# Performance work log

Measured on AMD Instinct MI355X. Metric: run time of the kernel, lower is better.

Reference implementation:

```python
import jax, jax.numpy as jnp
import numpy as np

NEG_SLOPE = 0.2
EPS = 1e-16

N_NODES = 50000
N_EDGES = 800000
IN_DIM = 64
HEADS = 4
HEAD_DIM = 64


def setup_inputs() -> dict:
    key = jax.random.key(0)
    k1, k2, k3, k4, k5 = jax.random.split(key, 5)
    x = jax.random.normal(k1, (N_NODES, IN_DIM), dtype=jnp.float32)
    edge_index = jax.random.randint(k2, (2, N_EDGES), 0, N_NODES, dtype=jnp.int64)
    W = jax.random.normal(k3, (IN_DIM, HEADS * HEAD_DIM), dtype=jnp.float32) * (1.0 / np.sqrt(IN_DIM))
    att_src = jax.random.normal(k4, (HEADS, HEAD_DIM), dtype=jnp.float32) * 0.1
    att_dst = jax.random.normal(k5, (HEADS, HEAD_DIM), dtype=jnp.float32) * 0.1
    bias = jnp.zeros((HEADS * HEAD_DIM,), dtype=jnp.float32)
    return {"x": x, "edge_index": edge_index, "W": W,
            "att_src": att_src, "att_dst": att_dst, "bias": bias}


def reference(x, edge_index, W, att_src, att_dst, bias):
    N = x.shape[0]
    H, D = att_src.shape
    # add self-loops (PyG default add_self_loops=True)
    loop = jnp.arange(N, dtype=edge_index.dtype)
    src = jnp.concatenate([edge_index[0], loop])  # message source j
    dst = jnp.concatenate([edge_index[1], loop])  # message target i

    h = (x @ W).reshape(N, H, D)                 # [N,H,D] per-head projection
    a_src = jnp.einsum('nhd,hd->nh', h, att_src)  # [N,H]
    a_dst = jnp.einsum('nhd,hd->nh', h, att_dst)  # [N,H]

    score = jax.nn.leaky_relu(a_src[src] + a_dst[dst], NEG_SLOPE)  # [E,H]
    # segment softmax over edges grouped by destination node
    m = jax.ops.segment_max(score, dst, num_segments=N)            # [N,H]
    m = jnp.where(jnp.isfinite(m), m, 0.0)
    e = jnp.exp(score - m[dst])                                    # [E,H]
    denom = jax.ops.segment_sum(e, dst, num_segments=N)            # [N,H]
    alpha = e / (denom[dst] + EPS)                                 # [E,H]

    msgs = h[src] * alpha[:, :, None]                              # [E,H,D]
    out = jax.ops.segment_sum(msgs, dst, num_segments=N)           # [N,H,D]
    return out.reshape(N, H * D) + bias
```

## Files before the change

kernel.cpp:

```cpp
#include <hip/hip_runtime.h>

#define N_NODES 50000
#define N_EDGES 800000
#define E_TOT   850000
#define HD      256
#define MAXDEG  64
#define NEG_SLOPE 0.2f
#define EPS 1e-16f

#define NB     98
#define BSHIFT 9
#define CAP    10240
#define ABLK   392
#define EPB    2304

typedef __attribute__((ext_vector_type(8))) short short8;
typedef __attribute__((ext_vector_type(4))) float f32x4;

__device__ __forceinline__ unsigned short f2bf(float f) {
    union { float f; unsigned int i; } c; c.f = f;
    unsigned int r = 0x7fffu + ((c.i >> 16) & 1u);
    return (unsigned short)((c.i + r) >> 16);
}
__device__ __forceinline__ float bf2f(unsigned short u) {
    union { unsigned int i; float f; } c; c.i = ((unsigned int)u) << 16;
    return c.f;
}
__device__ __forceinline__ short8 pack8(float4 a, float4 b) {
    short8 r;
    r[0] = (short)f2bf(a.x); r[1] = (short)f2bf(a.y);
    r[2] = (short)f2bf(a.z); r[3] = (short)f2bf(a.w);
    r[4] = (short)f2bf(b.x); r[5] = (short)f2bf(b.y);
    r[6] = (short)f2bf(b.z); r[7] = (short)f2bf(b.w);
    return r;
}
__device__ __forceinline__ float lrelu_exp(float v) {
    v = (v < 0.f) ? v * NEG_SLOPE : v;
    return __expf(v);
}

__global__ __launch_bounds__(256) void prep_kernel(
        const float* __restrict__ W, const float* __restrict__ att_src,
        const float* __restrict__ att_dst, float* __restrict__ ws, float* __restrict__ wd) {
    const int t = threadIdx.x, head = t >> 6, k = t & 63;
    const float* wrow = W + k * 256 + head * 64;
    const float* as = att_src + head * 64;
    const float* adv = att_dst + head * 64;
    float s = 0.f, d = 0.f;
#pragma unroll 8
    for (int j = 0; j < 64; ++j) { s += wrow[j] * as[j]; d += wrow[j] * adv[j]; }
    ws[k * 4 + head] = s;
    wd[k * 4 + head] = d;
}

__global__ __launch_bounds__(256) void bin_logit_kernel(
        const float* __restrict__ x,
        const float4* __restrict__ ws4, const float4* __restrict__ wd4,
        const int* __restrict__ eidx,
        int* __restrict__ gcnt, unsigned int* __restrict__ arena,
        float4* __restrict__ a_src4, float4* __restrict__ a_dst4,
        unsigned short* __restrict__ xb) {
    __shared__ int hist[NB];
    __shared__ int abase[NB];
    const int t = threadIdx.x;
    const int e0 = blockIdx.x * EPB;
    if (t < NB) hist[t] = 0;
    __syncthreads();

#pragma unroll
    for (int k = 0; k < EPB / 256; ++k) {
        const int g = e0 + k * 256 + t;
        if (g < E_TOT) {
            const int d = (g < N_EDGES) ? eidx[N_EDGES + g] : g - N_EDGES;
            atomicAdd(&hist[d >> BSHIFT], 1);
        }
    }
    __syncthreads();
    if (t < NB) {
        const int c = hist[t];
        abase[t] = c ? atomicAdd(&gcnt[t], c) : 0;
        hist[t] = 0;
    }
    __syncthreads();

#pragma unroll
    for (int k = 0; k < EPB / 256; ++k) {
        const int g = e0 + k * 256 + t;
        if (g < E_TOT) {
            int s, d;
            if (g < N_EDGES) { s = eidx[g]; d = eidx[N_EDGES + g]; }
            else             { s = d = g - N_EDGES; }
            const int b = d >> BSHIFT;
            const int pos = abase[b] + atomicAdd(&hist[b], 1);
            if (pos < CAP)
                arena[b * CAP + pos] =
                    (unsigned int)s | ((unsigned int)(d & 511) << 16);
        }
    }

    const int g = blockIdx.x * 256 + t;
    if (g < N_NODES) {
        const float4* xr = (const float4*)(x + (size_t)g * 64);
        float4 vs = {0.f, 0.f, 0.f, 0.f};
        float4 vd = {0.f, 0.f, 0.f, 0.f};
#pragma unroll 4
        for (int kk = 0; kk < 16; kk += 2) {
            float4 xv0 = xr[kk];
            float4 xv1 = xr[kk + 1];
            *(short8*)&xb[(size_t)g * 64 + kk * 4] = pack8(xv0, xv1);
#pragma unroll
            for (int j = 0; j < 8; ++j) {
                const float4 xv = (j < 4) ? xv0 : xv1;
                const int jj = j & 3;
                const float xj = jj == 0 ? xv.x : jj == 1 ? xv.y : jj == 2 ? xv.z : xv.w;
                const float4 w1 = ws4[(kk + (j >> 2)) * 4 + jj];
                const float4 w2 = wd4[(kk + (j >> 2)) * 4 + jj];
                vs.x += xj * w1.x; vs.y += xj * w1.y; vs.z += xj * w1.z; vs.w += xj * w1.w;
                vd.x += xj * w2.x; vd.y += xj * w2.y; vd.z += xj * w2.z; vd.w += xj * w2.w;
            }
        }
        a_src4[g] = vs;
        a_dst4[g] = vd;
    }
}

__global__ __launch_bounds__(512) void ell_build_kernel(
        const int* __restrict__ gcnt, const unsigned int* __restrict__ arena,
        int* __restrict__ cnt, unsigned short* __restrict__ slotu) {
    __shared__ int lcnt[512];
    const int t = threadIdx.x;
    const int b = blockIdx.x;
    lcnt[t] = 0;
    __syncthreads();
    int m = gcnt[b]; if (m > CAP) m = CAP;
    const int n0 = b << BSHIFT;
    const unsigned int* ap = arena + (size_t)b * CAP;
    for (int i = t; i < m; i += 512) {
        const unsigned int p = ap[i];
        const int dl = p >> 16;
        const int s  = p & 0xFFFFu;
        const int pos = atomicAdd(&lcnt[dl], 1);
        if (pos < MAXDEG) slotu[(size_t)(n0 + dl) * MAXDEG + pos] = (unsigned short)s;
    }
    __syncthreads();
    const int n = n0 + t;
    if (n < N_NODES) cnt[n] = lcnt[t];
}

__global__ __launch_bounds__(256) void aggregate_x_kernel(
        const int* __restrict__ cnt, const unsigned short* __restrict__ slotu,
        const float4* __restrict__ a_src4, const float4* __restrict__ a_dst4,
        const unsigned short* __restrict__ xb, unsigned short* __restrict__ yb) {
    __shared__ int    lsrc[4][64];
    __shared__ float4 lscs[4][64];
    const int w    = threadIdx.x >> 6;
    const int lane = threadIdx.x & 63;
    const int node = blockIdx.x * 4 + w;
    int deg = cnt[node];
    if (deg > MAXDEG) deg = MAXDEG;
    const size_t base = (size_t)node * MAXDEG;
    const float4 ad = a_dst4[node];

    int s = (lane < deg) ? (int)slotu[base + lane] : 0;
    float4 A = a_src4[s];
    float4 sc;
    if (lane < deg) {
        sc.x = lrelu_exp(A.x + ad.x); sc.y = lrelu_exp(A.y + ad.y);
        sc.z = lrelu_exp(A.z + ad.z); sc.w = lrelu_exp(A.w + ad.w);
    } else {
        sc = (float4){0.f, 0.f, 0.f, 0.f};
    }
    lsrc[w][lane] = s;
    lscs[w][lane] = sc;

    float4 ds = sc;
#pragma unroll
    for (int m = 1; m < 64; m <<= 1) {
        ds.x += __shfl_xor(ds.x, m, 64); ds.y += __shfl_xor(ds.y, m, 64);
        ds.z += __shfl_xor(ds.z, m, 64); ds.w += __shfl_xor(ds.w, m, 64);
    }
    float4 inv;
    inv.x = 1.f / (ds.x + EPS); inv.y = 1.f / (ds.y + EPS);
    inv.z = 1.f / (ds.z + EPS); inv.w = 1.f / (ds.w + EPS);

    float4 acc = {0.f, 0.f, 0.f, 0.f};
    int e = 0;
    for (; e + 3 < deg; e += 4) {
        int s0 = lsrc[w][e + 0], s1 = lsrc[w][e + 1];
        int s2 = lsrc[w][e + 2], s3 = lsrc[w][e + 3];
        float4 c0 = lscs[w][e + 0], c1 = lscs[w][e + 1];
        float4 c2 = lscs[w][e + 2], c3 = lscs[w][e + 3];
        float x0 = bf2f(xb[(size_t)s0 * 64 + lane]);
        float x1 = bf2f(xb[(size_t)s1 * 64 + lane]);
        float x2 = bf2f(xb[(size_t)s2 * 64 + lane]);
        float x3 = bf2f(xb[(size_t)s3 * 64 + lane]);
        acc.x += x0 * c0.x + x1 * c1.x + x2 * c2.x + x3 * c3.x;
        acc.y += x0 * c0.y + x1 * c1.y + x2 * c2.y + x3 * c3.y;
        acc.z += x0 * c0.z + x1 * c1.z + x2 * c2.z + x3 * c3.z;
        acc.w += x0 * c0.w + x1 * c1.w + x2 * c2.w + x3 * c3.w;
    }
    for (; e < deg; ++e) {
        int se = lsrc[w][e];
        float4 ce = lscs[w][e];
        float xv = bf2f(xb[(size_t)se * 64 + lane]);
        acc.x += xv * ce.x; acc.y += xv * ce.y;
        acc.z += xv * ce.z; acc.w += xv * ce.w;
    }
    unsigned short* yp = yb + (size_t)node * 256 + lane;
    __builtin_nontemporal_store(f2bf(acc.x * inv.x), yp);
    __builtin_nontemporal_store(f2bf(acc.y * inv.y), yp + 64);
    __builtin_nontemporal_store(f2bf(acc.z * inv.z), yp + 128);
    __builtin_nontemporal_store(f2bf(acc.w * inv.w), yp + 192);
}

__global__ __launch_bounds__(256) void gemm_out_kernel(
        const unsigned short* __restrict__ yb, const float* __restrict__ W,
        const float* __restrict__ bias, float* __restrict__ out) {
    __shared__ __align__(16) unsigned short Wt[256 * 64];
    const int t = threadIdx.x;
    {
        const int c = t;
        for (int kg = 0; kg < 8; ++kg) {
            float4 lo, hi;
            lo.x = W[(kg * 8 + 0) * 256 + c]; lo.y = W[(kg * 8 + 1) * 256 + c];
            lo.z = W[(kg * 8 + 2) * 256 + c]; lo.w = W[(kg * 8 + 3) * 256 + c];
            hi.x = W[(kg * 8 + 4) * 256 + c]; hi.y = W[(kg * 8 + 5) * 256 + c];
            hi.z = W[(kg * 8 + 6) * 256 + c]; hi.w = W[(kg * 8 + 7) * 256 + c];
            *(short8*)&Wt[c * 64 + ((kg ^ (c & 7)) << 3)] = pack8(lo, hi);
        }
    }
    __syncthreads();

    const int wave = t >> 6, lane = t & 63;
    const int q = lane >> 4, mloc = lane & 15;
    const int rowbase = blockIdx.x * 64 + wave * 16;
    int arow = rowbase + mloc;
    if (arow > N_NODES - 1) arow = N_NODES - 1;

    short8 a0[4], a1[4];
#pragma unroll
    for (int h = 0; h < 4; ++h) {
        const unsigned short* yr = yb + (size_t)arow * 256 + h * 64;
        a0[h] = *(const short8*)&yr[q * 8];
        a1[h] = *(const short8*)&yr[32 + q * 8];
    }

    f32x4 acc[16];
#pragma unroll
    for (int n = 0; n < 16; ++n) acc[n] = (f32x4){0.f, 0.f, 0.f, 0.f};
#pragma unroll
    for (int n = 0; n < 16; ++n) {
        const int c = n * 16 + mloc;
        const int h = n >> 2;
        const unsigned short* rowp = &Wt[c * 64];
        short8 b0 = *(const short8*)&rowp[((q    ) ^ (c & 7)) << 3];
        short8 b1 = *(const short8*)&rowp[((4 + q) ^ (c & 7)) << 3];
        acc[n] = __builtin_amdgcn_mfma_f32_16x16x32_bf16(a0[h], b0, acc[n], 0, 0, 0);
        acc[n] = __builtin_amdgcn_mfma_f32_16x16x32_bf16(a1[h], b1, acc[n], 0, 0, 0);
    }

    float bv[16];
#pragma unroll
    for (int n = 0; n < 16; ++n) bv[n] = bias[n * 16 + mloc];

    const int orow = rowbase + q * 4;
#pragma unroll
    for (int r = 0; r < 4; ++r) {
        if (orow + r < N_NODES) {
            float* op = out + (size_t)(orow + r) * 256 + mloc;
#pragma unroll
            for (int n = 0; n < 16; ++n) op[n * 16] = acc[n][r] + bv[n];
        }
    }
}

extern "C" void kernel_launch(void* const* d_in, const int* in_sizes, int n_in,
                              void* d_out, int out_size, void* d_ws, size_t ws_size,
                              hipStream_t stream) {
    const float* x       = (const float*)d_in[0];
    const int*   eidx    = (const int*)  d_in[1];
    const float* W       = (const float*)d_in[2];
    const float* att_src = (const float*)d_in[3];
    const float* att_dst = (const float*)d_in[4];
    const float* bias    = (const float*)d_in[5];
    float* out = (float*)d_out;

    unsigned short* yb = (unsigned short*)d_ws;
    float* a_src = (float*)(yb + (size_t)N_NODES * HD);
    float* a_dst = a_src + N_NODES * 4;
    float* ws    = a_dst + N_NODES * 4;
    float* wd    = ws + 256;
    int*   cnt   = (int*)(wd + 256);
    int*   gcnt  = cnt + N_NODES;
    unsigned int*   arena = (unsigned int*)(gcnt + 128);
    unsigned short* slotu = (unsigned short*)(arena + NB * CAP);
    unsigned short* xb    = slotu + (size_t)N_NODES * MAXDEG;

    hipMemsetAsync(gcnt, 0, 128 * sizeof(int), stream);
    prep_kernel<<<1, 256, 0, stream>>>(W, att_src, att_dst, ws, wd);
    bin_logit_kernel<<<ABLK, 256, 0, stream>>>(
        x, (const float4*)ws, (const float4*)wd, eidx, gcnt, arena,
        (float4*)a_src, (float4*)a_dst, xb);
    ell_build_kernel<<<NB, 512, 0, stream>>>(gcnt, arena, cnt, slotu);
    aggregate_x_kernel<<<N_NODES / 4, 256, 0, stream>>>(
        cnt, slotu, (const float4*)a_src, (const float4*)a_dst, xb, yb);
    gemm_out_kernel<<<(N_NODES + 63) / 64, 256, 0, stream>>>(yb, W, bias, out);
}
```

Before: 171.4 us.

## Fold gcnt reset into prep kernel, per-wave histograms, wider ELL build, plain stores

Drops the separate memset launch by zeroing the global bin counters inside prep_kernel. Splits the shared-memory binning histograms per wavefront to cut LDS atomic contention, and widens ell_build to 1024 threads with uint4 arena loads. Also swaps the nontemporal stores of the bf16 intermediate for regular stores so it may stay in cache for the following GEMM. Per-wave histograms change the order of edges within a bin, so neighbour order in each slot list is no longer the same as before.

```diff
diff --git a/kernel.cpp b/kernel.cpp
--- a/kernel.cpp
+++ b/kernel.cpp
@@ -41,8 +41,10 @@
 
 __global__ __launch_bounds__(256) void prep_kernel(
         const float* __restrict__ W, const float* __restrict__ att_src,
-        const float* __restrict__ att_dst, float* __restrict__ ws, float* __restrict__ wd) {
+        const float* __restrict__ att_dst, float* __restrict__ ws, float* __restrict__ wd,
+        int* __restrict__ gcnt) {
     const int t = threadIdx.x, head = t >> 6, k = t & 63;
+    if (t < 128) gcnt[t] = 0;
     const float* wrow = W + k * 256 + head * 64;
     const float* as = att_src + head * 64;
     const float* adv = att_dst + head * 64;
@@ -60,11 +62,12 @@
         int* __restrict__ gcnt, unsigned int* __restrict__ arena,
         float4* __restrict__ a_src4, float4* __restrict__ a_dst4,
         unsigned short* __restrict__ xb) {
-    __shared__ int hist[NB];
-    __shared__ int abase[NB];
+    __shared__ int hist[4][NB];
+    __shared__ int abase[4][NB];
     const int t = threadIdx.x;
+    const int w = t >> 6;
     const int e0 = blockIdx.x * EPB;
-    if (t < NB) hist[t] = 0;
+    for (int i = t; i < 4 * NB; i += 256) ((int*)hist)[i] = 0;
     __syncthreads();
 
 #pragma unroll
@@ -72,14 +75,19 @@
         const int g = e0 + k * 256 + t;
         if (g < E_TOT) {
             const int d = (g < N_EDGES) ? eidx[N_EDGES + g] : g - N_EDGES;
-            atomicAdd(&hist[d >> BSHIFT], 1);
+            atomicAdd(&hist[w][d >> BSHIFT], 1);
         }
     }
     __syncthreads();
     if (t < NB) {
-        const int c = hist[t];
-        abase[t] = c ? atomicAdd(&gcnt[t], c) : 0;
-        hist[t] = 0;
+        const int c0 = hist[0][t], c1 = hist[1][t], c2 = hist[2][t], c3 = hist[3][t];
+        const int tot = c0 + c1 + c2 + c3;
+        const int base = tot ? atomicAdd(&gcnt[t], tot) : 0;
+        abase[0][t] = base;
+        abase[1][t] = base + c0;
+        abase[2][t] = base + c0 + c1;
+        abase[3][t] = base + c0 + c1 + c2;
+        hist[0][t] = 0; hist[1][t] = 0; hist[2][t] = 0; hist[3][t] = 0;
     }
     __syncthreads();
 
@@ -91,7 +99,7 @@
             if (g < N_EDGES) { s = eidx[g]; d = eidx[N_EDGES + g]; }
             else             { s = d = g - N_EDGES; }
             const int b = d >> BSHIFT;
-            const int pos = abase[b] + atomicAdd(&hist[b], 1);
+            const int pos = abase[w][b] + atomicAdd(&hist[w][b], 1);
             if (pos < CAP)
                 arena[b * CAP + pos] =
                     (unsigned int)s | ((unsigned int)(d & 511) << 16);
@@ -124,18 +132,31 @@
     }
 }
 
-__global__ __launch_bounds__(512) void ell_build_kernel(
+__global__ __launch_bounds__(1024) void ell_build_kernel(
         const int* __restrict__ gcnt, const unsigned int* __restrict__ arena,
         int* __restrict__ cnt, unsigned short* __restrict__ slotu) {
     __shared__ int lcnt[512];
     const int t = threadIdx.x;
     const int b = blockIdx.x;
-    lcnt[t] = 0;
+    if (t < 512) lcnt[t] = 0;
     __syncthreads();
     int m = gcnt[b]; if (m > CAP) m = CAP;
     const int n0 = b << BSHIFT;
     const unsigned int* ap = arena + (size_t)b * CAP;
-    for (int i = t; i < m; i += 512) {
+    const uint4* ap4 = (const uint4*)ap;
+    const int m4 = m >> 2;
+    for (int i = t; i < m4; i += 1024) {
+        const uint4 p4 = ap4[i];
+#pragma unroll
+        for (int j = 0; j < 4; ++j) {
+            const unsigned int p = j == 0 ? p4.x : j == 1 ? p4.y : j == 2 ? p4.z : p4.w;
+            const int dl = p >> 16;
+            const int s  = p & 0xFFFFu;
+            const int pos = atomicAdd(&lcnt[dl], 1);
+            if (pos < MAXDEG) slotu[(size_t)(n0 + dl) * MAXDEG + pos] = (unsigned short)s;
+        }
+    }
+    for (int i = (m4 << 2) + t; i < m; i += 1024) {
         const unsigned int p = ap[i];
         const int dl = p >> 16;
         const int s  = p & 0xFFFFu;
@@ -143,8 +164,10 @@
         if (pos < MAXDEG) slotu[(size_t)(n0 + dl) * MAXDEG + pos] = (unsigned short)s;
     }
     __syncthreads();
-    const int n = n0 + t;
-    if (n < N_NODES) cnt[n] = lcnt[t];
+    if (t < 512) {
+        const int n = n0 + t;
+        if (n < N_NODES) cnt[n] = lcnt[t];
+    }
 }
 
 __global__ __launch_bounds__(256) void aggregate_x_kernel(
@@ -207,10 +230,10 @@
         acc.z += xv * ce.z; acc.w += xv * ce.w;
     }
     unsigned short* yp = yb + (size_t)node * 256 + lane;
-    __builtin_nontemporal_store(f2bf(acc.x * inv.x), yp);
-    __builtin_nontemporal_store(f2bf(acc.y * inv.y), yp + 64);
-    __builtin_nontemporal_store(f2bf(acc.z * inv.z), yp + 128);
-    __builtin_nontemporal_store(f2bf(acc.w * inv.w), yp + 192);
+    yp[  0] = f2bf(acc.x * inv.x);
+    yp[ 64] = f2bf(acc.y * inv.y);
+    yp[128] = f2bf(acc.z * inv.z);
+    yp[192] = f2bf(acc.w * inv.w);
 }
 
 __global__ __launch_bounds__(256) void gemm_out_kernel(
@@ -296,12 +319,11 @@
     unsigned short* slotu = (unsigned short*)(arena + NB * CAP);
     unsigned short* xb    = slotu + (size_t)N_NODES * MAXDEG;
 
-    hipMemsetAsync(gcnt, 0, 128 * sizeof(int), stream);
-    prep_kernel<<<1, 256, 0, stream>>>(W, att_src, att_dst, ws, wd);
+    prep_kernel<<<1, 256, 0, stream>>>(W, att_src, att_dst, ws, wd, gcnt);
     bin_logit_kernel<<<ABLK, 256, 0, stream>>>(
         x, (const float4*)ws, (const float4*)wd, eidx, gcnt, arena,
         (float4*)a_src, (float4*)a_dst, xb);
-    ell_build_kernel<<<NB, 512, 0, stream>>>(gcnt, arena, cnt, slotu);
+    ell_build_kernel<<<NB, 1024, 0, stream>>>(gcnt, arena, cnt, slotu);
     aggregate_x_kernel<<<N_NODES / 4, 256, 0, stream>>>(
         cnt, slotu, (const float4*)a_src, (const float4*)a_dst, xb, yb);
     gemm_out_kernel<<<(N_NODES + 63) / 64, 256, 0, stream>>>(yb, W, bias, out);
```

Result: faster. 167.4 us (-2.3%).
